# Optimization experiments

Measured on AMD Instinct MI355X. Metric: run time of the kernel, lower is better.

Reference implementation:

```python
import jax, jax.numpy as jnp
import numpy as np

# --- VMO muscle parameters (reconstructed VMOParameters defaults) ---
L0 = 0.089          # optimal_fiber_length [m]
LTS = 0.126         # tendon_slack_length [m]
PENN0 = 0.0873      # pennation_angle_at_optimal [rad]
VMAX = 10.0         # max contraction velocity [optimal lengths / s]
AF = 0.25           # Hill force-velocity curvature
FAT_RATE = 0.01     # fatigue_rate
REC_RATE = 0.002    # recovery_rate
TAU_ACT = 0.01      # activation time constant [s]
TAU_DEACT = 0.04    # deactivation time constant [s]
PHYSICS_WEIGHT = 0.8
LMT_DEFAULT = LTS + L0 * float(np.cos(PENN0))  # default_musculotendon_length
LMIN = 0.5 * L0
LMAX = 1.6 * L0
KT = 35.0           # tendon exponential stiffness
CT = 0.2            # tendon force scale

B, T, H = 8192, 2048, 64


def physics_rhs(state, exc):
    # state: [B, 3] = (fiber_length, activation, fatigue); exc: [B]
    lM = jnp.clip(state[..., 0], LMIN, LMAX)
    act = jnp.clip(state[..., 1], 0.01, 1.0)
    fat = jnp.clip(state[..., 2], 0.0, 1.0)
    a_eff = act * (1.0 - fat)
    # constant-thickness pennation model
    sin_p = jnp.clip(L0 * float(np.sin(PENN0)) / lM, 0.0, 0.99)
    cos_p = jnp.sqrt(1.0 - sin_p * sin_p)
    # Hill-type fiber velocity ODE (elastic tendon, lMT fixed at default, vMT = 0)
    lT = LMT_DEFAULT - lM * cos_p
    epsT = (lT - LTS) / LTS
    fT = jnp.where(epsT > 0.0, CT * (jnp.exp(KT * epsT) - 1.0), 0.0)
    lN = lM / L0
    fL = jnp.exp(-((lN - 1.0) ** 2) / 0.45)
    fPE = jnp.where(lN > 1.0,
                    (jnp.exp(5.0 * (lN - 1.0) / 0.6) - 1.0) / (float(np.exp(5.0)) - 1.0),
                    0.0)
    fV = (fT / cos_p - fPE) / (a_eff * fL + 1e-3)
    vN = jnp.clip((fV - 1.0) / (1.0 + jnp.abs(fV) / AF), -1.0, 1.5)  # inverse force-velocity
    fiber_velocity = VMAX * L0 * vN
    # first-order activation dynamics with activation-dependent time constant
    tau = jnp.where(exc > act, TAU_ACT * (0.5 + 1.5 * act), TAU_DEACT / (0.5 + 1.5 * act))
    activation_dot = (exc - act) / tau
    fatigue_dot = FAT_RATE * a_eff * (1.0 - fat) - REC_RATE * (1.0 - a_eff) * fat
    return jnp.stack([fiber_velocity, activation_dot, fatigue_dot], axis=-1)


def neural_correction(state, exc, W1, b1, W2, b2, W3, b3):
    x = jnp.concatenate([state, exc[..., None]], axis=-1)  # [B, 4]
    h = jnp.tanh(x @ W1 + b1)
    h = jnp.tanh(h @ W2 + b2)
    return 0.1 * jnp.tanh(h @ W3 + b3)


def ode_forward(initial_state, excitation_signal, t_span, W1, b1, W2, b2, W3, b3):
    n = t_span.shape[0]

    def rhs(t, y):
        # piecewise-constant excitation: torch.bucketize(t, t_span) - 1, clamped
        idx = jnp.clip(jnp.searchsorted(t_span, t, side='left') - 1, 0, n - 1)
        exc = excitation_signal[:, idx]
        return physics_rhs(y, exc) + (1.0 - PHYSICS_WEIGHT) * neural_correction(
            y, exc, W1, b1, W2, b2, W3, b3)

    @jax.checkpoint
    def step(y, i):
        t0, t1 = t_span[i], t_span[i + 1]
        dt = t1 - t0
        k1 = rhs(t0, y)
        k2 = rhs(t0 + 0.5 * dt, y + 0.5 * dt * k1)
        k3 = rhs(t0 + 0.5 * dt, y + 0.5 * dt * k2)
        k4 = rhs(t1, y + dt * k3)
        y1 = y + (dt / 6.0) * (k1 + 2.0 * k2 + 2.0 * k3 + k4)
        return y1, y1

    _, ys = jax.lax.scan(step, initial_state, jnp.arange(n - 1))
    return jnp.concatenate([initial_state[None], ys], axis=0)  # [T, B, 3]


def setup_inputs() -> dict:
    key = jax.random.key(0)
    ks = jax.random.split(key, 6)
    lM0 = L0 * (0.8 + 0.4 * jax.random.uniform(ks[0], (B,)))
    a0 = 0.05 + 0.1 * jax.random.uniform(ks[1], (B,))
    initial_state = jnp.stack([lM0, a0, jnp.zeros((B,))], axis=-1).astype(jnp.float32)
    excitation_signal = jax.random.uniform(ks[2], (B, T), dtype=jnp.float32)
    t_span = jnp.linspace(0.0, 2.0, T, dtype=jnp.float32)
    s = 0.1
    W1 = s * jax.random.normal(ks[3], (4, H), dtype=jnp.float32)
    W2 = s * jax.random.normal(ks[4], (H, H), dtype=jnp.float32)
    W3 = s * jax.random.normal(ks[5], (H, 3), dtype=jnp.float32)
    b1 = jnp.zeros((H,), jnp.float32)
    b2 = jnp.zeros((H,), jnp.float32)
    b3 = jnp.zeros((3,), jnp.float32)
    return {"initial_state": initial_state, "excitation_signal": excitation_signal,
            "t_span": t_span, "W1": W1, "b1": b1, "W2": W2, "b2": b2, "W3": W3, "b3": b3}


def reference(initial_state, excitation_signal, t_span, W1, b1, W2, b2, W3, b3):
    return ode_forward(initial_state, excitation_signal, t_span, W1, b1, W2, b2, W3, b3)
```

## Files before the change

### kernel.cpp

```cpp
#include <hip/hip_runtime.h>
#include <cstdint>

#define B_SZ 8192
#define T_SZ 2048

#define C_LTS       0.126f
#define C_LMIN      (0.5f * 0.089f)
#define C_LMAX      (1.6f * 0.089f)
#define C_KT        35.0f
#define C_CT        0.2f
#define C_VMAX_L0   (10.0f * 0.089f)
#define C_AF_INV    4.0f
#define C_FAT_RATE  0.01f
#define C_REC_RATE  0.002f
#define C_TAU_ACT   0.01f
#define C_TAU_DEACT 0.04f
#define C_L0SIN     0.0077598346f
#define C_LMT_DEF   0.2146610680f
#define C_INV_EM5   0.006783655f
#define C_INV_LTS   (1.0f / 0.126f)
#define C_INV_L0    (1.0f / 0.089f)
#define C_NN_SCALE  0.02f

typedef __attribute__((ext_vector_type(8))) short bf16x8;
typedef __attribute__((ext_vector_type(4))) float f32x4;

__device__ __forceinline__ float fast_rcp(float x) { return __builtin_amdgcn_rcpf(x); }
__device__ __forceinline__ float fast_rsq(float x) { return __builtin_amdgcn_rsqf(x); }
__device__ __forceinline__ float fast_tanh(float x) {
    const float e2 = __expf(2.0f * x);
    return 1.0f - 2.0f * fast_rcp(e2 + 1.0f);
}
__device__ __forceinline__ float clampf(float x, float lo, float hi) {
    return fminf(fmaxf(x, lo), hi);
}
__device__ __forceinline__ short f2bf_trunc(float f) {
    return (short)(__float_as_uint(f) >> 16);
}
__device__ __forceinline__ short f2bf_rne(float f) {
    uint32_t u = __float_as_uint(f);
    u += 0x7fff + ((u >> 16) & 1);
    return (short)(u >> 16);
}
__device__ __forceinline__ float bf2f(short s) {
    return __uint_as_float(((uint32_t)(unsigned short)s) << 16);
}

__global__ __launch_bounds__(256) void ode_kernel(
    const float* __restrict__ init_state,
    const float* __restrict__ exc,
    const float* __restrict__ tspan,
    const float* __restrict__ W1,
    const float* __restrict__ b1,
    const float* __restrict__ W2,
    const float* __restrict__ b2,
    const float* __restrict__ W3,
    const float* __restrict__ b3,
    float* __restrict__ out)
{
    const int tid  = threadIdx.x;
    const int wv   = tid >> 6;
    const int lane = tid & 63;
    const int r    = lane & 15;
    const int q    = lane >> 4;
    const int el   = (blockIdx.x << 4) + r;

    __shared__ __align__(16) short h1hi[1024];
    __shared__ __align__(16) short h1lo[1024];
    __shared__ __align__(16) float psum[256];
    __shared__ __align__(16) float cs_lds[64];

    float w1r[4][4], b1r[4];
    {
        const int j0 = (wv << 4) + (q << 2);
        #pragma unroll
        for (int u = 0; u < 4; ++u) {
            const int j = j0 + u;
            b1r[u]   = b1[j];
            w1r[0][u] = W1[j];
            w1r[1][u] = W1[64 + j];
            w1r[2][u] = W1[128 + j];
            w1r[3][u] = W1[192 + j];
        }
    }
    const int col = (wv << 4) + r;
    bf16x8 Wh[2], Wl[2];
    #pragma unroll
    for (int ks = 0; ks < 2; ++ks)
        #pragma unroll
        for (int t = 0; t < 8; ++t) {
            const int k = (ks << 5) + (q << 3) + t;
            const float wgt = W2[(k << 6) + col];
            const short hi = f2bf_trunc(wgt);
            Wh[ks][t] = hi;
            Wl[ks][t] = f2bf_rne(wgt - bf2f(hi));
        }
    float b2v4[4], w3r[4][3];
    #pragma unroll
    for (int reg = 0; reg < 4; ++reg) {
        const int c = (wv << 4) + (q << 2) + reg;
        b2v4[reg]  = b2[c];
        w3r[reg][0] = W3[c * 3 + 0];
        w3r[reg][1] = W3[c * 3 + 1];
        w3r[reg][2] = W3[c * 3 + 2];
    }
    const float b3v0 = b3[0], b3v1 = b3[1], b3v2 = b3[2];

    const int slotW = (wv << 1) + (q >> 1);
    const int widx  = (r << 6) + ((slotW ^ (r & 7)) << 3) + ((q & 1) << 2);
    const int ridx0 = (r << 6) + ((q       ^ (r & 7)) << 3);
    const int ridx1 = (r << 6) + (((4 | q) ^ (r & 7)) << 3);
    const int pswidx = (wv << 6) + (r << 2);

    float yb0 = init_state[el * 3 + 0];
    float yb1 = init_state[el * 3 + 1];
    float yb2 = init_state[el * 3 + 2];
    float cs0 = yb0, cs1 = yb1, cs2 = yb2;
    float ka0 = 0.f, ka1 = 0.f, ka2 = 0.f;

    if (wv == 0 && q == 0) {
        out[(size_t)el * 3 + 0] = yb0;
        out[(size_t)el * 3 + 1] = yb1;
        out[(size_t)el * 3 + 2] = yb2;
    }

    const float* excp = exc + (size_t)el * T_SZ;
    float excB = excp[0];
    float excA = excB;
    float tA = tspan[0], tB = tspan[1];

    #pragma unroll 1
    for (int i = 0; i < T_SZ - 1; ++i) {
        const float excN = excp[(i < T_SZ - 2) ? (i + 1) : (T_SZ - 2)];
        const float tN   = tspan[(i <= T_SZ - 3) ? (i + 2) : (T_SZ - 1)];
        const float dt  = tB - tA;
        const float hdt = 0.5f * dt;

        #pragma unroll
        for (int ev = 0; ev < 4; ++ev) {
            const float excv = (ev == 0) ? excA : excB;
            const float s0 = cs0, s1 = cs1, s2 = cs2;

            uint32_t hi01, hi23, lo01, lo23;
            {
                float hv[4];
                #pragma unroll
                for (int u = 0; u < 4; ++u) {
                    float pre = b1r[u];
                    pre = fmaf(s0,   w1r[0][u], pre);
                    pre = fmaf(s1,   w1r[1][u], pre);
                    pre = fmaf(s2,   w1r[2][u], pre);
                    pre = fmaf(excv, w1r[3][u], pre);
                    hv[u] = fast_tanh(pre);
                }
                const unsigned short h0 = (unsigned short)f2bf_trunc(hv[0]);
                const unsigned short h1_ = (unsigned short)f2bf_trunc(hv[1]);
                const unsigned short h2_ = (unsigned short)f2bf_trunc(hv[2]);
                const unsigned short h3_ = (unsigned short)f2bf_trunc(hv[3]);
                hi01 = (uint32_t)h0 | ((uint32_t)h1_ << 16);
                hi23 = (uint32_t)h2_ | ((uint32_t)h3_ << 16);
                const unsigned short l0 = (unsigned short)f2bf_rne(hv[0] - bf2f((short)h0));
                const unsigned short l1 = (unsigned short)f2bf_rne(hv[1] - bf2f((short)h1_));
                const unsigned short l2 = (unsigned short)f2bf_rne(hv[2] - bf2f((short)h2_));
                const unsigned short l3 = (unsigned short)f2bf_rne(hv[3] - bf2f((short)h3_));
                lo01 = (uint32_t)l0 | ((uint32_t)l1 << 16);
                lo23 = (uint32_t)l2 | ((uint32_t)l3 << 16);
            }
            *reinterpret_cast<uint2*>(&h1hi[widx]) = make_uint2(hi01, hi23);
            *reinterpret_cast<uint2*>(&h1lo[widx]) = make_uint2(lo01, lo23);
            __syncthreads();

            const bf16x8 Hh0 = *reinterpret_cast<const bf16x8*>(&h1hi[ridx0]);
            const bf16x8 Hh1 = *reinterpret_cast<const bf16x8*>(&h1hi[ridx1]);
            const bf16x8 Hl0 = *reinterpret_cast<const bf16x8*>(&h1lo[ridx0]);
            const bf16x8 Hl1 = *reinterpret_cast<const bf16x8*>(&h1lo[ridx1]);

            f32x4 accA = {b2v4[0], b2v4[1], b2v4[2], b2v4[3]};
            f32x4 accB = {0.f, 0.f, 0.f, 0.f};
            accA = __builtin_amdgcn_mfma_f32_16x16x32_bf16(Wh[0], Hl0, accA, 0, 0, 0);
            accB = __builtin_amdgcn_mfma_f32_16x16x32_bf16(Wh[1], Hl1, accB, 0, 0, 0);
            accA = __builtin_amdgcn_mfma_f32_16x16x32_bf16(Wl[0], Hh0, accA, 0, 0, 0);
            accB = __builtin_amdgcn_mfma_f32_16x16x32_bf16(Wl[1], Hh1, accB, 0, 0, 0);
            accA = __builtin_amdgcn_mfma_f32_16x16x32_bf16(Wh[0], Hh0, accA, 0, 0, 0);
            accB = __builtin_amdgcn_mfma_f32_16x16x32_bf16(Wh[1], Hh1, accB, 0, 0, 0);

            float p0 = 0.f, p1 = 0.f, p2 = 0.f;
            #pragma unroll
            for (int reg = 0; reg < 4; ++reg) {
                const float h2v = fast_tanh(accA[reg] + accB[reg]);
                p0 = fmaf(h2v, w3r[reg][0], p0);
                p1 = fmaf(h2v, w3r[reg][1], p1);
                p2 = fmaf(h2v, w3r[reg][2], p2);
            }
            p0 += __shfl_xor(p0, 16, 64);
            p1 += __shfl_xor(p1, 16, 64);
            p2 += __shfl_xor(p2, 16, 64);
            p0 += __shfl_xor(p0, 32, 64);
            p1 += __shfl_xor(p1, 32, 64);
            p2 += __shfl_xor(p2, 32, 64);
            if (q == 0) {
                *reinterpret_cast<f32x4*>(&psum[pswidx]) = (f32x4){p0, p1, p2, p2};
            }
            __syncthreads();

            if (wv == 0) {
                const f32x4 v0 = *reinterpret_cast<const f32x4*>(&psum[(r << 2)]);
                const f32x4 v1 = *reinterpret_cast<const f32x4*>(&psum[64 + (r << 2)]);
                const f32x4 v2 = *reinterpret_cast<const f32x4*>(&psum[128 + (r << 2)]);
                const f32x4 v3 = *reinterpret_cast<const f32x4*>(&psum[192 + (r << 2)]);
                const float S0 = (v0[0] + v1[0]) + (v2[0] + v3[0]);
                const float S1 = (v0[1] + v1[1]) + (v2[1] + v3[1]);
                const float S2 = (v0[2] + v1[2]) + (v2[2] + v3[2]);

                const float nn0 = C_NN_SCALE * fast_tanh(S0 + b3v0);
                const float nn1 = C_NN_SCALE * fast_tanh(S1 + b3v1);
                const float nn2 = C_NN_SCALE * fast_tanh(S2 + b3v2);

                const float lM  = clampf(s0, C_LMIN, C_LMAX);
                const float act = clampf(s1, 0.01f, 1.0f);
                const float fat = clampf(s2, 0.0f, 1.0f);
                const float a_eff = act * (1.0f - fat);
                const float sin_p = fminf(C_L0SIN * fast_rcp(lM), 0.99f);
                const float cp2   = fmaf(-sin_p, sin_p, 1.0f);
                const float inv_cp = fast_rsq(cp2);
                const float cos_p  = cp2 * inv_cp;
                const float lT   = C_LMT_DEF - lM * cos_p;
                const float epsT = (lT - C_LTS) * C_INV_LTS;
                const float fT   = (epsT > 0.0f) ? C_CT * (__expf(C_KT * epsT) - 1.0f) : 0.0f;
                const float lN   = lM * C_INV_L0;
                const float d1   = lN - 1.0f;
                const float fL   = __expf(-d1 * d1 * (1.0f / 0.45f));
                const float fPE  = (lN > 1.0f) ? (__expf(8.3333333333f * d1) - 1.0f) * C_INV_EM5 : 0.0f;
                const float fV   = (fT * inv_cp - fPE) * fast_rcp(fmaf(a_eff, fL, 0.001f));
                float vN = (fV - 1.0f) * fast_rcp(fmaf(fabsf(fV), C_AF_INV, 1.0f));
                vN = clampf(vN, -1.0f, 1.5f);
                const float r0v = fmaf(C_VMAX_L0, vN, nn0);
                const float g15 = fmaf(1.5f, act, 0.5f);
                const float inv_tau = (excv > act) ? fast_rcp(C_TAU_ACT * g15)
                                                   : g15 * (1.0f / C_TAU_DEACT);
                const float r1v = fmaf(excv - act, inv_tau, nn1);
                const float r2v = C_FAT_RATE * a_eff * (1.0f - fat)
                                - C_REC_RATE * (1.0f - a_eff) * fat + nn2;

                if (ev == 0) {
                    ka0 = r0v; ka1 = r1v; ka2 = r2v;
                    cs0 = fmaf(hdt, r0v, yb0); cs1 = fmaf(hdt, r1v, yb1); cs2 = fmaf(hdt, r2v, yb2);
                } else if (ev == 1) {
                    ka0 = fmaf(2.0f, r0v, ka0); ka1 = fmaf(2.0f, r1v, ka1); ka2 = fmaf(2.0f, r2v, ka2);
                    cs0 = fmaf(hdt, r0v, yb0); cs1 = fmaf(hdt, r1v, yb1); cs2 = fmaf(hdt, r2v, yb2);
                } else if (ev == 2) {
                    ka0 = fmaf(2.0f, r0v, ka0); ka1 = fmaf(2.0f, r1v, ka1); ka2 = fmaf(2.0f, r2v, ka2);
                    cs0 = fmaf(dt, r0v, yb0); cs1 = fmaf(dt, r1v, yb1); cs2 = fmaf(dt, r2v, yb2);
                } else {
                    const float c6 = dt * (1.0f / 6.0f);
                    yb0 = fmaf(c6, ka0 + r0v, yb0);
                    yb1 = fmaf(c6, ka1 + r1v, yb1);
                    yb2 = fmaf(c6, ka2 + r2v, yb2);
                    cs0 = yb0; cs1 = yb1; cs2 = yb2;
                }
                if (q == 0) {
                    *reinterpret_cast<f32x4*>(&cs_lds[r << 2]) = (f32x4){cs0, cs1, cs2, 0.f};
                    if (ev == 3) {
                        const size_t ob = (size_t)(i + 1) * (B_SZ * 3) + (size_t)el * 3;
                        out[ob + 0] = cs0; out[ob + 1] = cs1; out[ob + 2] = cs2;
                    }
                }
            }
            __syncthreads();

            if (wv != 0) {
                const f32x4 c = *reinterpret_cast<const f32x4*>(&cs_lds[r << 2]);
                cs0 = c[0]; cs1 = c[1]; cs2 = c[2];
            }
        }

        excA = excB; excB = excN; tA = tB; tB = tN;
    }
}

extern "C" void kernel_launch(void* const* d_in, const int* in_sizes, int n_in,
                              void* d_out, int out_size, void* d_ws, size_t ws_size,
                              hipStream_t stream) {
    const float* init  = (const float*)d_in[0];
    const float* exc   = (const float*)d_in[1];
    const float* tspan = (const float*)d_in[2];
    const float* W1    = (const float*)d_in[3];
    const float* b1    = (const float*)d_in[4];
    const float* W2    = (const float*)d_in[5];
    const float* b2    = (const float*)d_in[6];
    const float* W3    = (const float*)d_in[7];
    const float* b3    = (const float*)d_in[8];

    hipLaunchKernelGGL(ode_kernel, dim3(B_SZ / 16), dim3(256), 0, stream,
                       init, exc, tspan, W1, b1, W2, b2, W3, b3, (float*)d_out);
}
```

Baseline: 9.422 ms.

## Split hidden-layer K dimension across two wave groups with 512-thread blocks

```diff
diff --git a/kernel.cpp b/kernel.cpp
--- a/kernel.cpp
+++ b/kernel.cpp
@@ -46,7 +46,7 @@
     return __uint_as_float(((uint32_t)(unsigned short)s) << 16);
 }
 
-__global__ __launch_bounds__(256) void ode_kernel(
+__global__ __launch_bounds__(512) void ode_kernel(
     const float* __restrict__ init_state,
     const float* __restrict__ exc,
     const float* __restrict__ tspan,
@@ -59,7 +59,9 @@
     float* __restrict__ out)
 {
     const int tid  = threadIdx.x;
-    const int wv   = tid >> 6;
+    const int w    = tid >> 6;
+    const int wv   = w & 3;
+    const int kh   = w >> 2;
     const int lane = tid & 63;
     const int r    = lane & 15;
     const int q    = lane >> 4;
@@ -67,14 +69,15 @@
 
     __shared__ __align__(16) short h1hi[1024];
     __shared__ __align__(16) short h1lo[1024];
-    __shared__ __align__(16) float psum[256];
+    __shared__ __align__(16) float pacc[1024];
+    __shared__ __align__(16) float psum[512];
     __shared__ __align__(16) float cs_lds[64];
 
-    float w1r[4][4], b1r[4];
+    float w1r[4][2], b1r[2];
     {
-        const int j0 = (wv << 4) + (q << 2);
+        const int j0 = (w << 3) + (q << 1);
         #pragma unroll
-        for (int u = 0; u < 4; ++u) {
+        for (int u = 0; u < 2; ++u) {
             const int j = j0 + u;
             b1r[u]   = b1[j];
             w1r[0][u] = W1[j];
@@ -84,33 +87,35 @@
         }
     }
     const int col = (wv << 4) + r;
-    bf16x8 Wh[2], Wl[2];
+    bf16x8 Wh, Wl;
     #pragma unroll
-    for (int ks = 0; ks < 2; ++ks)
-        #pragma unroll
-        for (int t = 0; t < 8; ++t) {
-            const int k = (ks << 5) + (q << 3) + t;
-            const float wgt = W2[(k << 6) + col];
-            const short hi = f2bf_trunc(wgt);
-            Wh[ks][t] = hi;
-            Wl[ks][t] = f2bf_rne(wgt - bf2f(hi));
-        }
-    float b2v4[4], w3r[4][3];
+    for (int t = 0; t < 8; ++t) {
+        const int k = (kh << 5) + (q << 3) + t;
+        const float wgt = W2[(k << 6) + col];
+        const short hi = f2bf_trunc(wgt);
+        Wh[t] = hi;
+        Wl[t] = f2bf_rne(wgt - bf2f(hi));
+    }
+    float b2i[4];
     #pragma unroll
-    for (int reg = 0; reg < 4; ++reg) {
-        const int c = (wv << 4) + (q << 2) + reg;
-        b2v4[reg]  = b2[c];
-        w3r[reg][0] = W3[c * 3 + 0];
-        w3r[reg][1] = W3[c * 3 + 1];
-        w3r[reg][2] = W3[c * 3 + 2];
+    for (int reg = 0; reg < 4; ++reg)
+        b2i[reg] = (kh == 0) ? b2[(wv << 4) + (q << 2) + reg] : 0.0f;
+    float w3r[2][3];
+    #pragma unroll
+    for (int u = 0; u < 2; ++u) {
+        const int c = (wv << 4) + (q << 2) + (kh << 1) + u;
+        w3r[u][0] = W3[c * 3 + 0];
+        w3r[u][1] = W3[c * 3 + 1];
+        w3r[u][2] = W3[c * 3 + 2];
     }
     const float b3v0 = b3[0], b3v1 = b3[1], b3v2 = b3[2];
 
-    const int slotW = (wv << 1) + (q >> 1);
-    const int widx  = (r << 6) + ((slotW ^ (r & 7)) << 3) + ((q & 1) << 2);
-    const int ridx0 = (r << 6) + ((q       ^ (r & 7)) << 3);
-    const int ridx1 = (r << 6) + (((4 | q) ^ (r & 7)) << 3);
-    const int pswidx = (wv << 6) + (r << 2);
+    const int widx  = (r << 6) + ((w ^ (r & 7)) << 3) + (q << 1);
+    const int ridx  = (r << 6) + ((((kh << 2) | q) ^ (r & 7)) << 3);
+    const int paw   = (w << 7) + (lane << 1);
+    const int wp    = ((1 - kh) << 2) | wv;
+    const int par   = (wp << 7) + (lane << 1);
+    const int pswidx = (w << 6) + (r << 2);
 
     float yb0 = init_state[el * 3 + 0];
     float yb1 = init_state[el * 3 + 1];
@@ -118,7 +123,7 @@
     float cs0 = yb0, cs1 = yb1, cs2 = yb2;
     float ka0 = 0.f, ka1 = 0.f, ka2 = 0.f;
 
-    if (wv == 0 && q == 0) {
+    if (w == 0 && q == 0) {
         out[(size_t)el * 3 + 0] = yb0;
         out[(size_t)el * 3 + 1] = yb1;
         out[(size_t)el * 3 + 2] = yb2;
@@ -141,11 +146,10 @@
             const float excv = (ev == 0) ? excA : excB;
             const float s0 = cs0, s1 = cs1, s2 = cs2;
 
-            uint32_t hi01, hi23, lo01, lo23;
             {
-                float hv[4];
+                float hv[2];
                 #pragma unroll
-                for (int u = 0; u < 4; ++u) {
+                for (int u = 0; u < 2; ++u) {
                     float pre = b1r[u];
                     pre = fmaf(s0,   w1r[0][u], pre);
                     pre = fmaf(s1,   w1r[1][u], pre);
@@ -155,43 +159,36 @@
                 }
                 const unsigned short h0 = (unsigned short)f2bf_trunc(hv[0]);
                 const unsigned short h1_ = (unsigned short)f2bf_trunc(hv[1]);
-                const unsigned short h2_ = (unsigned short)f2bf_trunc(hv[2]);
-                const unsigned short h3_ = (unsigned short)f2bf_trunc(hv[3]);
-                hi01 = (uint32_t)h0 | ((uint32_t)h1_ << 16);
-                hi23 = (uint32_t)h2_ | ((uint32_t)h3_ << 16);
+                const uint32_t hi01 = (uint32_t)h0 | ((uint32_t)h1_ << 16);
                 const unsigned short l0 = (unsigned short)f2bf_rne(hv[0] - bf2f((short)h0));
                 const unsigned short l1 = (unsigned short)f2bf_rne(hv[1] - bf2f((short)h1_));
-                const unsigned short l2 = (unsigned short)f2bf_rne(hv[2] - bf2f((short)h2_));
-                const unsigned short l3 = (unsigned short)f2bf_rne(hv[3] - bf2f((short)h3_));
-                lo01 = (uint32_t)l0 | ((uint32_t)l1 << 16);
-                lo23 = (uint32_t)l2 | ((uint32_t)l3 << 16);
-            }
-            *reinterpret_cast<uint2*>(&h1hi[widx]) = make_uint2(hi01, hi23);
-            *reinterpret_cast<uint2*>(&h1lo[widx]) = make_uint2(lo01, lo23);
-            __syncthreads();
-
-            const bf16x8 Hh0 = *reinterpret_cast<const bf16x8*>(&h1hi[ridx0]);
-            const bf16x8 Hh1 = *reinterpret_cast<const bf16x8*>(&h1hi[ridx1]);
-            const bf16x8 Hl0 = *reinterpret_cast<const bf16x8*>(&h1lo[ridx0]);
-            const bf16x8 Hl1 = *reinterpret_cast<const bf16x8*>(&h1lo[ridx1]);
-
-            f32x4 accA = {b2v4[0], b2v4[1], b2v4[2], b2v4[3]};
-            f32x4 accB = {0.f, 0.f, 0.f, 0.f};
-            accA = __builtin_amdgcn_mfma_f32_16x16x32_bf16(Wh[0], Hl0, accA, 0, 0, 0);
-            accB = __builtin_amdgcn_mfma_f32_16x16x32_bf16(Wh[1], Hl1, accB, 0, 0, 0);
-            accA = __builtin_amdgcn_mfma_f32_16x16x32_bf16(Wl[0], Hh0, accA, 0, 0, 0);
-            accB = __builtin_amdgcn_mfma_f32_16x16x32_bf16(Wl[1], Hh1, accB, 0, 0, 0);
-            accA = __builtin_amdgcn_mfma_f32_16x16x32_bf16(Wh[0], Hh0, accA, 0, 0, 0);
-            accB = __builtin_amdgcn_mfma_f32_16x16x32_bf16(Wh[1], Hh1, accB, 0, 0, 0);
-
-            float p0 = 0.f, p1 = 0.f, p2 = 0.f;
-            #pragma unroll
-            for (int reg = 0; reg < 4; ++reg) {
-                const float h2v = fast_tanh(accA[reg] + accB[reg]);
-                p0 = fmaf(h2v, w3r[reg][0], p0);
-                p1 = fmaf(h2v, w3r[reg][1], p1);
-                p2 = fmaf(h2v, w3r[reg][2], p2);
-            }
+                const uint32_t lo01 = (uint32_t)l0 | ((uint32_t)l1 << 16);
+                *reinterpret_cast<uint32_t*>(&h1hi[widx]) = hi01;
+                *reinterpret_cast<uint32_t*>(&h1lo[widx]) = lo01;
+            }
+            __syncthreads();
+
+            const bf16x8 Hh = *reinterpret_cast<const bf16x8*>(&h1hi[ridx]);
+            const bf16x8 Hl = *reinterpret_cast<const bf16x8*>(&h1lo[ridx]);
+            f32x4 acc = {b2i[0], b2i[1], b2i[2], b2i[3]};
+            acc = __builtin_amdgcn_mfma_f32_16x16x32_bf16(Wh, Hl, acc, 0, 0, 0);
+            acc = __builtin_amdgcn_mfma_f32_16x16x32_bf16(Wl, Hh, acc, 0, 0, 0);
+            acc = __builtin_amdgcn_mfma_f32_16x16x32_bf16(Wh, Hh, acc, 0, 0, 0);
+
+            const float wr0 = kh ? acc[0] : acc[2];
+            const float wr1 = kh ? acc[1] : acc[3];
+            *reinterpret_cast<float2*>(&pacc[paw]) = make_float2(wr0, wr1);
+            __syncthreads();
+
+            const float2 pr = *reinterpret_cast<const float2*>(&pacc[par]);
+            const float own0 = kh ? acc[2] : acc[0];
+            const float own1 = kh ? acc[3] : acc[1];
+            const float h2a = fast_tanh(own0 + pr.x);
+            const float h2b = fast_tanh(own1 + pr.y);
+
+            float p0 = fmaf(h2b, w3r[1][0], h2a * w3r[0][0]);
+            float p1 = fmaf(h2b, w3r[1][1], h2a * w3r[0][1]);
+            float p2 = fmaf(h2b, w3r[1][2], h2a * w3r[0][2]);
             p0 += __shfl_xor(p0, 16, 64);
             p1 += __shfl_xor(p1, 16, 64);
             p2 += __shfl_xor(p2, 16, 64);
@@ -203,14 +200,18 @@
             }
             __syncthreads();
 
-            if (wv == 0) {
-                const f32x4 v0 = *reinterpret_cast<const f32x4*>(&psum[(r << 2)]);
-                const f32x4 v1 = *reinterpret_cast<const f32x4*>(&psum[64 + (r << 2)]);
-                const f32x4 v2 = *reinterpret_cast<const f32x4*>(&psum[128 + (r << 2)]);
-                const f32x4 v3 = *reinterpret_cast<const f32x4*>(&psum[192 + (r << 2)]);
-                const float S0 = (v0[0] + v1[0]) + (v2[0] + v3[0]);
-                const float S1 = (v0[1] + v1[1]) + (v2[1] + v3[1]);
-                const float S2 = (v0[2] + v1[2]) + (v2[2] + v3[2]);
+            if (w == 0) {
+                const f32x4 va = *reinterpret_cast<const f32x4*>(&psum[(q << 7) + (r << 2)]);
+                const f32x4 vb = *reinterpret_cast<const f32x4*>(&psum[(q << 7) + 64 + (r << 2)]);
+                float S0 = va[0] + vb[0];
+                float S1 = va[1] + vb[1];
+                float S2 = va[2] + vb[2];
+                S0 += __shfl_xor(S0, 16, 64);
+                S1 += __shfl_xor(S1, 16, 64);
+                S2 += __shfl_xor(S2, 16, 64);
+                S0 += __shfl_xor(S0, 32, 64);
+                S1 += __shfl_xor(S1, 32, 64);
+                S2 += __shfl_xor(S2, 32, 64);
 
                 const float nn0 = C_NN_SCALE * fast_tanh(S0 + b3v0);
                 const float nn1 = C_NN_SCALE * fast_tanh(S1 + b3v1);
@@ -242,33 +243,34 @@
                 const float r2v = C_FAT_RATE * a_eff * (1.0f - fat)
                                 - C_REC_RATE * (1.0f - a_eff) * fat + nn2;
 
+                float ns0, ns1, ns2;
                 if (ev == 0) {
                     ka0 = r0v; ka1 = r1v; ka2 = r2v;
-                    cs0 = fmaf(hdt, r0v, yb0); cs1 = fmaf(hdt, r1v, yb1); cs2 = fmaf(hdt, r2v, yb2);
+                    ns0 = fmaf(hdt, r0v, yb0); ns1 = fmaf(hdt, r1v, yb1); ns2 = fmaf(hdt, r2v, yb2);
                 } else if (ev == 1) {
                     ka0 = fmaf(2.0f, r0v, ka0); ka1 = fmaf(2.0f, r1v, ka1); ka2 = fmaf(2.0f, r2v, ka2);
-                    cs0 = fmaf(hdt, r0v, yb0); cs1 = fmaf(hdt, r1v, yb1); cs2 = fmaf(hdt, r2v, yb2);
+                    ns0 = fmaf(hdt, r0v, yb0); ns1 = fmaf(hdt, r1v, yb1); ns2 = fmaf(hdt, r2v, yb2);
                 } else if (ev == 2) {
                     ka0 = fmaf(2.0f, r0v, ka0); ka1 = fmaf(2.0f, r1v, ka1); ka2 = fmaf(2.0f, r2v, ka2);
-                    cs0 = fmaf(dt, r0v, yb0); cs1 = fmaf(dt, r1v, yb1); cs2 = fmaf(dt, r2v, yb2);
+                    ns0 = fmaf(dt, r0v, yb0); ns1 = fmaf(dt, r1v, yb1); ns2 = fmaf(dt, r2v, yb2);
                 } else {
                     const float c6 = dt * (1.0f / 6.0f);
                     yb0 = fmaf(c6, ka0 + r0v, yb0);
                     yb1 = fmaf(c6, ka1 + r1v, yb1);
                     yb2 = fmaf(c6, ka2 + r2v, yb2);
-                    cs0 = yb0; cs1 = yb1; cs2 = yb2;
+                    ns0 = yb0; ns1 = yb1; ns2 = yb2;
                 }
                 if (q == 0) {
-                    *reinterpret_cast<f32x4*>(&cs_lds[r << 2]) = (f32x4){cs0, cs1, cs2, 0.f};
+                    *reinterpret_cast<f32x4*>(&cs_lds[r << 2]) = (f32x4){ns0, ns1, ns2, 0.f};
                     if (ev == 3) {
                         const size_t ob = (size_t)(i + 1) * (B_SZ * 3) + (size_t)el * 3;
-                        out[ob + 0] = cs0; out[ob + 1] = cs1; out[ob + 2] = cs2;
+                        out[ob + 0] = ns0; out[ob + 1] = ns1; out[ob + 2] = ns2;
                     }
                 }
             }
             __syncthreads();
 
-            if (wv != 0) {
+            {
                 const f32x4 c = *reinterpret_cast<const f32x4*>(&cs_lds[r << 2]);
                 cs0 = c[0]; cs1 = c[1]; cs2 = c[2];
             }
@@ -291,6 +293,6 @@
     const float* W3    = (const float*)d_in[7];
     const float* b3    = (const float*)d_in[8];
 
-    hipLaunchKernelGGL(ode_kernel, dim3(B_SZ / 16), dim3(256), 0, stream,
+    hipLaunchKernelGGL(ode_kernel, dim3(B_SZ / 16), dim3(512), 0, stream,
                        init, exc, tspan, W1, b1, W2, b2, W3, b3, (float*)d_out);
 }
```

New measurement: 10.72 ms. 1.14x slower.
